# Optimization experiments

Hardware: AMD Instinct MI355X
Metric: run time of the kernel (lower is better)

Reference implementation:

```python
import jax, jax.numpy as jnp
import numpy as np

L, D, F, H = 6, 512, 2048, 8
DH = D // H
SCALE = DH ** -0.5
B, S = 2, 2048


def _ln(x, w, b):
    m = jnp.mean(x, axis=-1, keepdims=True)
    v = jnp.var(x, axis=-1, keepdims=True)
    return (x - m) * jax.lax.rsqrt(v + 1e-5) * w + b


def setup_inputs() -> dict:
    key = jax.random.key(0)
    ks = jax.random.split(key, 10)
    s = 0.02
    return {
        "x": jax.random.normal(ks[0], (B, S, D), jnp.float32),
        "mask": jnp.zeros((B, 1, 1, S), jnp.float32),
        "ln1_w": jnp.ones((L, D), jnp.float32),
        "ln1_b": jnp.zeros((L, D), jnp.float32),
        "in_w": s * jax.random.normal(ks[1], (L, D, 3 * D), jnp.float32),
        "in_b": jnp.zeros((L, 3 * D), jnp.float32),
        "out_w": s * jax.random.normal(ks[2], (L, D, D), jnp.float32),
        "out_b": jnp.zeros((L, D), jnp.float32),
        "ln2_w": jnp.ones((L, D), jnp.float32),
        "ln2_b": jnp.zeros((L, D), jnp.float32),
        "ffn1_w": s * jax.random.normal(ks[3], (L, D, F), jnp.float32),
        "ffn1_b": jnp.zeros((L, F), jnp.float32),
        "ffn2_w": s * jax.random.normal(ks[4], (L, F, D), jnp.float32),
        "ffn2_b": jnp.zeros((L, D), jnp.float32),
        "norm_w": jnp.ones((D,), jnp.float32),
        "norm_b": jnp.zeros((D,), jnp.float32),
    }


def reference(x, mask, ln1_w, ln1_b, in_w, in_b, out_w, out_b,
              ln2_w, ln2_b, ffn1_w, ffn1_b, ffn2_w, ffn2_b, norm_w, norm_b):
    def step(h, p):
        (l1w, l1b, iw, ib, ow, ob, l2w, l2b, f1w, f1b, f2w, f2b) = p
        # --- self-attention (pre-norm) ---
        y = _ln(h, l1w, l1b)
        proj = y @ iw + ib                       # [B,S,3D]
        q, k, v = jnp.split(proj, 3, axis=-1)    # each [B,S,D]
        q = q.reshape(B, S, H, DH)
        k = k.reshape(B, S, H, DH)
        v = v.reshape(B, S, H, DH)
        dot = jnp.einsum('bqhd,bkhd->bhqk', q * SCALE, k) + mask  # [B,H,S,S]
        att = jax.nn.softmax(dot, axis=-1)
        o = jnp.einsum('bhqk,bkhd->bqhd', att, v).reshape(B, S, D)
        h = o @ ow + ob + h
        # --- FFN (pre-norm) ---
        y = _ln(h, l2w, l2b)
        y = jax.nn.relu(y @ f1w + f1b) @ f2w + f2b
        return h + y, None

    params = (ln1_w, ln1_b, in_w, in_b, out_w, out_b,
              ln2_w, ln2_b, ffn1_w, ffn1_b, ffn2_w, ffn2_b)
    x, _ = jax.lax.scan(step, x, params)
    return _ln(x, norm_w, norm_b)
```

## Files before the change

### kernel.cpp

```cpp
#include <hip/hip_runtime.h>
#include <hip/hip_bf16.h>
#include <stdint.h>


typedef __bf16 bf16x8 __attribute__((ext_vector_type(8)));
typedef __bf16 bf16x4 __attribute__((ext_vector_type(4)));
typedef float f32x4 __attribute__((ext_vector_type(4)));
typedef unsigned short u16;
typedef unsigned short u16x8 __attribute__((ext_vector_type(8)));

#define NB 2
#define NS 2048
#define ND 512
#define NH 8
#define NDH 64
#define NF 2048
#define NL 6
#define NCHUNK 4
#define CK (NS / NCHUNK)
#define LOG2E 1.4426950408889634f
#define QSCALE (0.125f * LOG2E)

#if defined(__has_builtin)
#if __has_builtin(__builtin_amdgcn_global_load_lds)
#define HAVE_GLDS 1
#endif
#endif
#ifndef HAVE_GLDS
#define HAVE_GLDS 0
#endif

#if HAVE_GLDS
__device__ __forceinline__ void glds16(const u16* g, u16* l) {
  __builtin_amdgcn_global_load_lds(
      (const __attribute__((address_space(1))) unsigned int*)g,
      (__attribute__((address_space(3))) unsigned int*)l, 16, 0, 0);
}
#endif

__device__ __forceinline__ u16 f2bf(float f) {
  unsigned u = __float_as_uint(f);
  u += 0x7FFFu + ((u >> 16) & 1u);
  return (u16)(u >> 16);
}

__global__ __launch_bounds__(256) void wcvt_t(const float* __restrict__ src,
                                              u16* __restrict__ dst,
                                              int K, int N) {
  __shared__ float tile[32][33];
  int l = blockIdx.z;
  const float* s = src + (size_t)l * K * N;
  u16* d = dst + (size_t)l * K * N;
  int k0 = blockIdx.y * 32, n0 = blockIdx.x * 32;
  int tx = threadIdx.x, ty = threadIdx.y;
  for (int i = 0; i < 32; i += 8)
    tile[ty + i][tx] = s[(size_t)(k0 + ty + i) * N + n0 + tx];
  __syncthreads();
  for (int i = 0; i < 32; i += 8)
    d[(size_t)(n0 + ty + i) * K + k0 + tx] = f2bf(tile[tx][ty + i]);
}

template <int OUT_BF16>
__global__ __launch_bounds__(256) void ln_k(const float* __restrict__ x,
                                            const float* __restrict__ w,
                                            const float* __restrict__ b,
                                            void* __restrict__ out) {
  int row = blockIdx.x;
  int t = threadIdx.x;
  const float* xr = x + (size_t)row * ND;
  float2 v = ((const float2*)xr)[t];
  float s = v.x + v.y, ss = v.x * v.x + v.y * v.y;
  for (int o = 32; o > 0; o >>= 1) {
    s += __shfl_down(s, o);
    ss += __shfl_down(ss, o);
  }
  __shared__ float rs[4], rss[4];
  if ((t & 63) == 0) { rs[t >> 6] = s; rss[t >> 6] = ss; }
  __syncthreads();
  float S = rs[0] + rs[1] + rs[2] + rs[3];
  float SS = rss[0] + rss[1] + rss[2] + rss[3];
  float mean = S * (1.0f / ND);
  float var = SS * (1.0f / ND) - mean * mean;
  float rstd = rsqrtf(var + 1e-5f);
  float2 wv = ((const float2*)w)[t];
  float2 bv = ((const float2*)b)[t];
  float y0 = (v.x - mean) * rstd * wv.x + bv.x;
  float y1 = (v.y - mean) * rstd * wv.y + bv.y;
  if (OUT_BF16) {
    ushort2 p; p.x = f2bf(y0); p.y = f2bf(y1);
    ((ushort2*)out)[(size_t)row * (ND / 2) + t] = p;
  } else {
    float2 p; p.x = y0; p.y = y1;
    ((float2*)out)[(size_t)row * (ND / 2) + t] = p;
  }
}

template <int EPI, int BM, int BN, int BK>
__global__ __launch_bounds__(256) void gemm_bt(const u16* __restrict__ A,
                                               const u16* __restrict__ Bt,
                                               const float* __restrict__ bias,
                                               const float* __restrict__ resid,
                                               void* __restrict__ C,
                                               int M, int N, int K) {
  constexpr int MT = BM / 32;
  constexpr int NT = BN / 32;
  constexpr int CB = BK / 8;
  constexpr int RPP = 2048 / BK;
  constexpr int AP = BM / RPP;
  constexpr int BP = BN / RPP;
  constexpr int KK = BK / 32;
  __shared__ u16 la[BM * BK];
  __shared__ u16 lb[BN * BK];
  int bm = blockIdx.y, bn = blockIdx.x;
  int t = threadIdx.x;
  int wave = t >> 6, lane = t & 63, quad = lane >> 4, l15 = lane & 15;
  int wm = (wave >> 1) * (BM / 2), wn = (wave & 1) * (BN / 2);
  f32x4 acc[MT][NT] = {};
  int srow = t / CB;
  int scol = ((t % CB) ^ (srow & (CB - 1))) * 8;
  const u16* Ag = A + (size_t)(bm * BM) * K;
  const u16* Bg = Bt + (size_t)(bn * BN) * K;
#if HAVE_GLDS
  u16* laB = la + wave * 512;
  u16* lbB = lb + wave * 512;
#endif
  for (int k0 = 0; k0 < K; k0 += BK) {
    __syncthreads();
#if HAVE_GLDS
#pragma unroll
    for (int g = 0; g < AP; g++)
      glds16(&Ag[(size_t)(srow + g * RPP) * K + k0 + scol], laB + g * 2048);
#pragma unroll
    for (int g = 0; g < BP; g++)
      glds16(&Bg[(size_t)(srow + g * RPP) * K + k0 + scol], lbB + g * 2048);
#else
#pragma unroll
    for (int g = 0; g < AP; g++)
      *(bf16x8*)&la[(srow + g * RPP) * BK + (t % CB) * 8] =
          *(const bf16x8*)&Ag[(size_t)(srow + g * RPP) * K + k0 + scol];
#pragma unroll
    for (int g = 0; g < BP; g++)
      *(bf16x8*)&lb[(srow + g * RPP) * BK + (t % CB) * 8] =
          *(const bf16x8*)&Bg[(size_t)(srow + g * RPP) * K + k0 + scol];
#endif
    __syncthreads();
#pragma unroll
    for (int kk = 0; kk < KK; kk++) {
      bf16x8 af[MT], bfr[NT];
#pragma unroll
      for (int i = 0; i < MT; i++) {
        int row = wm + i * 16 + l15;
        af[i] = *(const bf16x8*)&la[row * BK + ((kk * 4 + quad) ^ (row & (CB - 1))) * 8];
      }
#pragma unroll
      for (int i = 0; i < NT; i++) {
        int row = wn + i * 16 + l15;
        bfr[i] = *(const bf16x8*)&lb[row * BK + ((kk * 4 + quad) ^ (row & (CB - 1))) * 8];
      }
#pragma unroll
      for (int mt = 0; mt < MT; mt++)
#pragma unroll
        for (int nt = 0; nt < NT; nt++)
          acc[mt][nt] = __builtin_amdgcn_mfma_f32_16x16x32_bf16(
              af[mt], bfr[nt], acc[mt][nt], 0, 0, 0);
    }
  }
#pragma unroll
  for (int mt = 0; mt < MT; mt++)
#pragma unroll
    for (int nt = 0; nt < NT; nt++) {
      int col = bn * BN + wn + nt * 16 + l15;
      float bcol = (EPI == 3) ? 0.f : bias[col];
#pragma unroll
      for (int r = 0; r < 4; r++) {
        int row = bm * BM + wm + mt * 16 + quad * 4 + r;
        float v = acc[mt][nt][r] + ((EPI == 3) ? bias[row] : bcol);
        if (EPI == 1) v = fmaxf(v, 0.f);
        if (EPI == 2)
          ((float*)C)[(size_t)row * N + col] = v + resid[(size_t)row * N + col];
        else
          ((u16*)C)[(size_t)row * N + col] = f2bf(v);
      }
    }
}

__global__ __launch_bounds__(256) void attn_k(const u16* __restrict__ qk,
                                              const u16* __restrict__ vt,
                                              const float* __restrict__ mask,
                                              u16* __restrict__ opart,
                                              float* __restrict__ lbuf) {
  __shared__ u16 kt_s[64 * 64];
  __shared__ u16 vt_s[64 * 64];
  __shared__ u16 p_s[4][16 * 68];
  int bh = blockIdx.y;
  int b = bh >> 3, h = bh & 7;
  int qt = blockIdx.x;
  int c = blockIdx.z;
  int t = threadIdx.x;
  int wave = t >> 6, lane = t & 63, quad = lane >> 4, l15 = lane & 15;

  int qrow = qt * 64 + wave * 16 + l15;
  const u16* qbase = qk + ((size_t)(b * NS + qrow)) * (2 * ND) + h * NDH;
  bf16x8 qf[2];
  qf[0] = *(const bf16x8*)&qbase[quad * 8];
  qf[1] = *(const bf16x8*)&qbase[32 + quad * 8];
#pragma unroll
  for (int e = 0; e < 8; e++) {
    qf[0][e] = (__bf16)((float)qf[0][e] * QSCALE);
    qf[1][e] = (__bf16)((float)qf[1][e] * QSCALE);
  }
  bf16x8 ones;
#pragma unroll
  for (int e = 0; e < 8; e++) ones[e] = (__bf16)1.0f;

  f32x4 oacc[4] = {};
  f32x4 ls = {};

  int srow8 = t >> 3;
  int segsw = ((t & 7) ^ ((t >> 3) & 7)) * 8;
  const u16* kg0 = qk + ((size_t)(b * NS + srow8)) * (2 * ND) + ND + h * NDH + segsw;
  const u16* vg0 = vt + ((size_t)(h * NDH + srow8)) * (NB * NS) + b * NS + segsw;
#if HAVE_GLDS
  u16* ktB = kt_s + wave * 512;
  u16* vtB = vt_s + wave * 512;
#endif
  for (int kt0 = c * CK; kt0 < (c + 1) * CK; kt0 += 64) {
    float m2[4];
#pragma unroll
    for (int nt = 0; nt < 4; nt++)
      m2[nt] = mask[b * NS + kt0 + nt * 16 + l15] * LOG2E;
    __syncthreads();
#if HAVE_GLDS
    glds16(&kg0[(size_t)kt0 * (2 * ND)], ktB);
    glds16(&kg0[(size_t)(kt0 + 32) * (2 * ND)], ktB + 2048);
    glds16(&vg0[kt0], vtB);
    glds16(&vg0[kt0 + (size_t)32 * (NB * NS)], vtB + 2048);
#else
    *(bf16x8*)&kt_s[srow8 * 64 + (t & 7) * 8] =
        *(const bf16x8*)&kg0[(size_t)kt0 * (2 * ND)];
    *(bf16x8*)&kt_s[(srow8 + 32) * 64 + (t & 7) * 8] =
        *(const bf16x8*)&kg0[(size_t)(kt0 + 32) * (2 * ND)];
    *(bf16x8*)&vt_s[srow8 * 64 + (t & 7) * 8] = *(const bf16x8*)&vg0[kt0];
    *(bf16x8*)&vt_s[(srow8 + 32) * 64 + (t & 7) * 8] =
        *(const bf16x8*)&vg0[kt0 + (size_t)32 * (NB * NS)];
#endif
    __syncthreads();
    f32x4 sc[4] = {};
#pragma unroll
    for (int nt = 0; nt < 4; nt++) {
      int row = nt * 16 + l15;
      bf16x8 kf0 = *(const bf16x8*)&kt_s[row * 64 + (quad ^ (row & 7)) * 8];
      bf16x8 kf1 = *(const bf16x8*)&kt_s[row * 64 + ((quad + 4) ^ (row & 7)) * 8];
      sc[nt] = __builtin_amdgcn_mfma_f32_16x16x32_bf16(qf[0], kf0, sc[nt], 0, 0, 0);
      sc[nt] = __builtin_amdgcn_mfma_f32_16x16x32_bf16(qf[1], kf1, sc[nt], 0, 0, 0);
    }
    u16* pw = &p_s[wave][0];
#pragma unroll
    for (int nt = 0; nt < 4; nt++) {
#pragma unroll
      for (int rp = 0; rp < 2; rp++) {
        float2 pp;
        pp.x = __builtin_amdgcn_exp2f(sc[nt][2 * rp] + m2[nt]);
        pp.y = __builtin_amdgcn_exp2f(sc[nt][2 * rp + 1] + m2[nt]);
        __hip_bfloat162 bb = __float22bfloat162_rn(pp);
        ushort2 us = *reinterpret_cast<ushort2*>(&bb);
        pw[(quad * 4 + 2 * rp) * 68 + nt * 16 + l15] = us.x;
        pw[(quad * 4 + 2 * rp + 1) * 68 + nt * 16 + l15] = us.y;
      }
    }
    asm volatile("s_waitcnt lgkmcnt(0)" ::: "memory");
#pragma unroll
    for (int kk = 0; kk < 2; kk++) {
      bf16x4 plo = *(const bf16x4*)&pw[l15 * 68 + kk * 32 + quad * 8];
      bf16x4 phi = *(const bf16x4*)&pw[l15 * 68 + kk * 32 + quad * 8 + 4];
      bf16x8 pf = __builtin_shufflevector(plo, phi, 0, 1, 2, 3, 4, 5, 6, 7);
#pragma unroll
      for (int nt = 0; nt < 4; nt++) {
        int row = nt * 16 + l15;
        bf16x8 vf = *(const bf16x8*)&vt_s[row * 64 + ((kk * 4 + quad) ^ (row & 7)) * 8];
        oacc[nt] = __builtin_amdgcn_mfma_f32_16x16x32_bf16(pf, vf, oacc[nt], 0, 0, 0);
      }
      ls = __builtin_amdgcn_mfma_f32_16x16x32_bf16(pf, ones, ls, 0, 0, 0);
    }
  }
  u16* ob = opart + (((size_t)(c * NB * NH + bh) * NS) + qt * 64 + wave * 16) * NDH;
#pragma unroll
  for (int nt = 0; nt < 4; nt++)
#pragma unroll
    for (int r = 0; r < 4; r++)
      ob[(size_t)(quad * 4 + r) * NDH + nt * 16 + l15] = f2bf(oacc[nt][r]);
  if (l15 == 0) {
    size_t li = (size_t)(c * NB * NH + bh) * NS + qt * 64 + wave * 16 + quad * 4;
#pragma unroll
    for (int r = 0; r < 4; r++) lbuf[li + r] = ls[r];
  }
}

__global__ __launch_bounds__(256) void attn_merge(const u16* __restrict__ opart,
                                                  const float* __restrict__ lbuf,
                                                  u16* __restrict__ o) {
  int gt = blockIdx.x * 256 + threadIdx.x;
  int grp = gt & 7;
  int s = (gt >> 3) & (NS - 1);
  int bh = gt >> 14;
  float L = 0.f;
#pragma unroll
  for (int c = 0; c < NCHUNK; c++)
    L += lbuf[(size_t)(c * NB * NH + bh) * NS + s];
  float inv = 1.0f / L;
  float acc[8] = {};
#pragma unroll
  for (int c = 0; c < NCHUNK; c++) {
    bf16x8 ov = *(const bf16x8*)&opart[((size_t)(c * NB * NH + bh) * NS + s) * NDH + grp * 8];
#pragma unroll
    for (int j = 0; j < 8; j++) acc[j] += (float)ov[j];
  }
  u16x8 res;
#pragma unroll
  for (int j = 0; j < 8; j++) res[j] = f2bf(acc[j] * inv);
  int b = bh >> 3, h = bh & 7;
  *(u16x8*)&o[((size_t)(b * NS + s)) * ND + h * NDH + grp * 8] = res;
}

extern "C" void kernel_launch(void* const* d_in, const int* in_sizes, int n_in,
                              void* d_out, int out_size, void* d_ws, size_t ws_size,
                              hipStream_t stream) {
  const float* x = (const float*)d_in[0];
  const float* mask = (const float*)d_in[1];
  const float* ln1w = (const float*)d_in[2];
  const float* ln1b = (const float*)d_in[3];
  const float* in_w = (const float*)d_in[4];
  const float* in_b = (const float*)d_in[5];
  const float* out_w = (const float*)d_in[6];
  const float* out_b = (const float*)d_in[7];
  const float* ln2w = (const float*)d_in[8];
  const float* ln2b = (const float*)d_in[9];
  const float* f1w = (const float*)d_in[10];
  const float* f1b = (const float*)d_in[11];
  const float* f2w = (const float*)d_in[12];
  const float* f2b = (const float*)d_in[13];
  const float* normw = (const float*)d_in[14];
  const float* normb = (const float*)d_in[15];

  char* ws = (char*)d_ws;
  auto carve = [&](size_t bytes) {
    char* p = ws;
    ws += (bytes + 255) & ~(size_t)255;
    return p;
  };
  u16* wq_t = (u16*)carve((size_t)NL * 3 * ND * ND * 2);
  u16* wo_t = (u16*)carve((size_t)NL * ND * ND * 2);
  u16* w1_t = (u16*)carve((size_t)NL * NF * ND * 2);
  u16* w2_t = (u16*)carve((size_t)NL * ND * NF * 2);
  u16* ybuf = (u16*)carve((size_t)NB * NS * ND * 2);
  u16* qk = (u16*)carve((size_t)NB * NS * 2 * ND * 2);
  u16* vtb = (u16*)carve((size_t)ND * NB * NS * 2);
  u16* obuf = (u16*)carve((size_t)NB * NS * ND * 2);
  u16* ubuf = (u16*)carve((size_t)NB * NS * NF * 2);
  float* hA = (float*)carve((size_t)NB * NS * ND * 4);
  float* hB = (float*)carve((size_t)NB * NS * ND * 4);
  float* lbuf = (float*)carve((size_t)NCHUNK * NB * NH * NS * 4);
  u16* opart = ubuf;

  const int M = NB * NS;
  dim3 tb(32, 8);
  wcvt_t<<<dim3(3 * ND / 32, ND / 32, NL), tb, 0, stream>>>(in_w, wq_t, ND, 3 * ND);
  wcvt_t<<<dim3(ND / 32, ND / 32, NL), tb, 0, stream>>>(out_w, wo_t, ND, ND);
  wcvt_t<<<dim3(NF / 32, ND / 32, NL), tb, 0, stream>>>(f1w, w1_t, ND, NF);
  wcvt_t<<<dim3(ND / 32, NF / 32, NL), tb, 0, stream>>>(f2w, w2_t, NF, ND);

  const float* hin = x;
  for (int l = 0; l < NL; l++) {
    ln_k<1><<<M, 256, 0, stream>>>(hin, ln1w + l * ND, ln1b + l * ND, ybuf);
    gemm_bt<0, 64, 128, 128><<<dim3(2 * ND / 128, M / 64), 256, 0, stream>>>(
        ybuf, wq_t + (size_t)l * 3 * ND * ND, in_b + l * 3 * ND, nullptr, qk,
        M, 2 * ND, ND);
    gemm_bt<3, 64, 64, 128><<<dim3(M / 64, ND / 64), 256, 0, stream>>>(
        wq_t + (size_t)l * 3 * ND * ND + (size_t)2 * ND * ND, ybuf,
        in_b + l * 3 * ND + 2 * ND, nullptr, vtb, ND, M, ND);
    attn_k<<<dim3(NS / 64, NB * NH, NCHUNK), 256, 0, stream>>>(
        qk, vtb, mask, opart, lbuf);
    attn_merge<<<(NB * NH * NS * 8) / 256, 256, 0, stream>>>(opart, lbuf, obuf);
    gemm_bt<2, 64, 64, 128><<<dim3(ND / 64, M / 64), 256, 0, stream>>>(
        obuf, wo_t + (size_t)l * ND * ND, out_b + l * ND, hin, hB, M, ND, ND);
    ln_k<1><<<M, 256, 0, stream>>>(hB, ln2w + l * ND, ln2b + l * ND, ybuf);
    gemm_bt<1, 128, 128, 64><<<dim3(NF / 128, M / 128), 256, 0, stream>>>(
        ybuf, w1_t + (size_t)l * NF * ND, f1b + l * NF, nullptr, ubuf, M, NF, ND);
    gemm_bt<2, 64, 64, 128><<<dim3(ND / 64, M / 64), 256, 0, stream>>>(
        ubuf, w2_t + (size_t)l * ND * NF, f2b + l * ND, hB, hA, M, ND, NF);
    hin = hA;
  }
  ln_k<0><<<M, 256, 0, stream>>>(hA, normw, normb, (float*)d_out);
}
```

Baseline: 830.6 us.

## Split-K the FFN2 GEMM with a reduction kernel and double attention chunks

```diff
diff --git a/kernel.cpp b/kernel.cpp
--- a/kernel.cpp
+++ b/kernel.cpp
@@ -16,7 +16,7 @@
 #define NDH 64
 #define NF 2048
 #define NL 6
-#define NCHUNK 4
+#define NCHUNK 8
 #define CK (NS / NCHUNK)
 #define LOG2E 1.4426950408889634f
 #define QSCALE (0.125f * LOG2E)
@@ -95,7 +95,7 @@
   }
 }
 
-template <int EPI, int BM, int BN, int BK>
+template <int EPI, int BM, int BN, int BK, int KSPLIT = 1>
 __global__ __launch_bounds__(256) void gemm_bt(const u16* __restrict__ A,
                                                const u16* __restrict__ Bt,
                                                const float* __restrict__ bias,
@@ -112,19 +112,22 @@
   __shared__ u16 la[BM * BK];
   __shared__ u16 lb[BN * BK];
   int bm = blockIdx.y, bn = blockIdx.x;
+  int kc = (KSPLIT > 1) ? blockIdx.z : 0;
+  int klen = K / KSPLIT;
+  int kbase = kc * klen;
   int t = threadIdx.x;
   int wave = t >> 6, lane = t & 63, quad = lane >> 4, l15 = lane & 15;
   int wm = (wave >> 1) * (BM / 2), wn = (wave & 1) * (BN / 2);
   f32x4 acc[MT][NT] = {};
   int srow = t / CB;
   int scol = ((t % CB) ^ (srow & (CB - 1))) * 8;
-  const u16* Ag = A + (size_t)(bm * BM) * K;
-  const u16* Bg = Bt + (size_t)(bn * BN) * K;
+  const u16* Ag = A + (size_t)(bm * BM) * K + kbase;
+  const u16* Bg = Bt + (size_t)(bn * BN) * K + kbase;
 #if HAVE_GLDS
   u16* laB = la + wave * 512;
   u16* lbB = lb + wave * 512;
 #endif
-  for (int k0 = 0; k0 < K; k0 += BK) {
+  for (int k0 = 0; k0 < klen; k0 += BK) {
     __syncthreads();
 #if HAVE_GLDS
 #pragma unroll
@@ -170,7 +173,7 @@
 #pragma unroll
     for (int nt = 0; nt < NT; nt++) {
       int col = bn * BN + wn + nt * 16 + l15;
-      float bcol = (EPI == 3) ? 0.f : bias[col];
+      float bcol = (EPI == 3 || EPI == 4) ? 0.f : bias[col];
 #pragma unroll
       for (int r = 0; r < 4; r++) {
         int row = bm * BM + wm + mt * 16 + quad * 4 + r;
@@ -178,10 +181,35 @@
         if (EPI == 1) v = fmaxf(v, 0.f);
         if (EPI == 2)
           ((float*)C)[(size_t)row * N + col] = v + resid[(size_t)row * N + col];
+        else if (EPI == 4)
+          ((u16*)C)[(size_t)kc * M * N + (size_t)row * N + col] = f2bf(v);
         else
           ((u16*)C)[(size_t)row * N + col] = f2bf(v);
       }
     }
+}
+
+__global__ __launch_bounds__(256) void ksplit_red(const u16* __restrict__ part,
+                                                  const float* __restrict__ bias,
+                                                  const float* __restrict__ resid,
+                                                  float* __restrict__ out) {
+  int gt = blockIdx.x * 256 + threadIdx.x;
+  int col = (gt & 63) * 8;
+  int row = gt >> 6;
+  size_t base = (size_t)row * ND + col;
+  float acc[8];
+#pragma unroll
+  for (int j = 0; j < 8; j++) acc[j] = bias[col + j] + resid[base + j];
+#pragma unroll
+  for (int c = 0; c < 4; c++) {
+    bf16x8 v = *(const bf16x8*)&part[(size_t)c * (NB * NS) * ND + base];
+#pragma unroll
+    for (int j = 0; j < 8; j++) acc[j] += (float)v[j];
+  }
+#pragma unroll
+  for (int j = 0; j < 2; j++)
+    *(float4*)&out[base + j * 4] =
+        make_float4(acc[j * 4], acc[j * 4 + 1], acc[j * 4 + 2], acc[j * 4 + 3]);
 }
 
 __global__ __launch_bounds__(256) void attn_k(const u16* __restrict__ qk,
@@ -360,7 +388,8 @@
   float* hA = (float*)carve((size_t)NB * NS * ND * 4);
   float* hB = (float*)carve((size_t)NB * NS * ND * 4);
   float* lbuf = (float*)carve((size_t)NCHUNK * NB * NH * NS * 4);
-  u16* opart = ubuf;
+  u16* opart = (u16*)carve((size_t)NCHUNK * NB * NH * NS * NDH * 2);
+  u16* pbuf = (u16*)carve((size_t)4 * NB * NS * ND * 2);
 
   const int M = NB * NS;
   dim3 tb(32, 8);
@@ -386,8 +415,10 @@
     ln_k<1><<<M, 256, 0, stream>>>(hB, ln2w + l * ND, ln2b + l * ND, ybuf);
     gemm_bt<1, 128, 128, 64><<<dim3(NF / 128, M / 128), 256, 0, stream>>>(
         ybuf, w1_t + (size_t)l * NF * ND, f1b + l * NF, nullptr, ubuf, M, NF, ND);
-    gemm_bt<2, 64, 64, 128><<<dim3(ND / 64, M / 64), 256, 0, stream>>>(
-        ubuf, w2_t + (size_t)l * ND * NF, f2b + l * ND, hB, hA, M, ND, NF);
+    gemm_bt<4, 128, 128, 64, 4><<<dim3(ND / 128, M / 128, 4), 256, 0, stream>>>(
+        ubuf, w2_t + (size_t)l * ND * NF, nullptr, nullptr, pbuf, M, ND, NF);
+    ksplit_red<<<(M * ND / 8) / 256, 256, 0, stream>>>(
+        pbuf, f2b + l * ND, hB, hA);
     hin = hA;
   }
   ln_k<0><<<M, 256, 0, stream>>>(hA, normw, normb, (float*)d_out);
```

After: 849.3 us. +2.3%, slower.
